# Kernel tuning notes

Hardware: AMD Instinct MI355X
Metric: run time of the kernel (lower is better)

Reference implementation:

```python
import jax, jax.numpy as jnp
import numpy as np

B, C, H, L, D = 128, 5, 50, 32, 300
VOCAB = 50000
KN = 20  # len(torch.arange(-0.9, 1.1, 0.1))
EPS = 1e-8


def setup_inputs() -> dict:
    key = jax.random.key(0)
    k1, k2, k3, k4 = jax.random.split(key, 4)
    return {
        "candidate_title": jax.random.randint(k1, (B, C, L), 0, VOCAB),
        "clicked_title": jax.random.randint(k2, (B, H, L), 0, VOCAB),
        "embedding": jax.random.normal(k3, (VOCAB, D), dtype=jnp.float32),
        "ltr_w": jax.random.normal(k4, (1, H * KN), dtype=jnp.float32) * 0.03,
        "ltr_b": jnp.zeros((1,), dtype=jnp.float32),
    }


def reference(candidate_title, clicked_title, embedding, ltr_w, ltr_b):
    mus = jnp.arange(KN, dtype=jnp.float32) * 0.1 - 0.9
    sigmas = jnp.concatenate([jnp.full((KN - 1,), 0.1, dtype=jnp.float32),
                              jnp.array([0.001], dtype=jnp.float32)])

    ce = embedding[candidate_title]            # [B,C,L,D]
    he = embedding[clicked_title]              # [B,H,L,D]
    # torch CosineSimilarity: dot / (clamp(||a||,eps)*clamp(||b||,eps))
    cn = ce / jnp.clip(jnp.linalg.norm(ce, axis=-1, keepdims=True), EPS)
    hn = he / jnp.clip(jnp.linalg.norm(he, axis=-1, keepdims=True), EPS)
    sim = jnp.einsum('bcid,bhjd->bchij', cn, hn)  # [B,C,H,L,L] fusion matrix

    # kernel pooling: sum over columns j per Gaussian kernel, then log-sum over rows i
    pooled = jnp.stack(
        [jnp.sum(jnp.exp(-(sim - mus[k]) ** 2 / (2.0 * sigmas[k] ** 2)), axis=-1)
         for k in range(KN)], axis=-1)          # [B,C,H,L,KN]
    pv = jnp.sum(jnp.log(jnp.clip(pooled, 1e-10)), axis=-2)  # [B,C,H,KN]
    pv = pv.reshape(B, C, H * KN)

    score = pv @ ltr_w.T + ltr_b               # [B,C,1]
    return jax.nn.log_softmax(score, axis=1)[..., 0]  # [B,C]
```

## Files before the change

kernel.cpp:

```cpp
#include <hip/hip_runtime.h>
#include <hip/hip_bf16.h>

#define VOCABN 50000
#define BN 128
#define CN 5
#define HN 50
#define LN 32
#define DN 300
#define DP 320
#define KNN 20

typedef __bf16    bf16x8 __attribute__((ext_vector_type(8)));
typedef float     f32x4  __attribute__((ext_vector_type(4)));
typedef float     f32x2  __attribute__((ext_vector_type(2)));
typedef ushort    u16x8  __attribute__((ext_vector_type(8)));

#if __has_builtin(__builtin_amdgcn_exp2f)
#define FEXP2 __builtin_amdgcn_exp2f
#else
#define FEXP2 exp2f
#endif
#if __has_builtin(__builtin_amdgcn_logf)
#define FLOG2 __builtin_amdgcn_logf
#else
#define FLOG2 log2f
#endif

#define LOG2E 1.4426950408889634f
#define LN2F  0.6931471805599453f

__global__ __launch_bounds__(256) void knorm_embed2(const float* __restrict__ emb,
                                                    ushort* __restrict__ tabo) {
    const int t    = threadIdx.x;
    const int lane = t & 63;
    const int w    = t >> 6;
    const int v    = blockIdx.x * 4 + w;
    const float* row = emb + (size_t)v * DN;
    const float4* r4 = (const float4*)row;

    float4 x = r4[lane];
    float ss = x.x * x.x + x.y * x.y + x.z * x.z + x.w * x.w;
    if (lane < 11) {
        float4 y = r4[64 + lane];
        ss += y.x * y.x + y.y * y.y + y.z * y.z + y.w * y.w;
    }
    #pragma unroll
    for (int off = 32; off; off >>= 1) ss += __shfl_xor(ss, off);
    const float scale = 1.0f / fmaxf(sqrtf(ss), 1e-8f);

    if (lane < 40) {
        u16x8 u;
        #pragma unroll
        for (int j = 0; j < 8; ++j) {
            int e = lane * 8 + j;
            float f = (e < DN) ? row[e] * scale : 0.f;
            __hip_bfloat16 h = __float2bfloat16(f);
            u[j] = *(ushort*)&h;
        }
        *(u16x8*)(tabo + (size_t)v * DP + lane * 8) = u;
    }
}

__device__ __forceinline__ int paddr(int row, int c) {
    return ((row >> 1) << 7) + ((((c + ((row & 1) << 2))) ^ ((row >> 1) & 7)) << 4);
}
__device__ __forceinline__ bf16x8 ldP(const ushort* buf, int row, int c) {
    return *(const bf16x8*)((const char*)buf + paddr(row, c));
}

__global__ __launch_bounds__(320, 6) void knrm_fused9(const int* __restrict__ cand,
                                                      const int* __restrict__ clik,
                                                      const ushort* __restrict__ tab,
                                                      const float* __restrict__ ltr_w,
                                                      float* __restrict__ score) {
    __shared__ __align__(16) char smem[25984];
    ushort* Bbuf0 = (ushort*)(smem + 21120);
    ushort* Bbuf1 = (ushort*)(smem + 23168);
    int*    tokA  = (int*)(smem + 25216);
    int*    tokB  = (int*)(smem + 25856);

    const int t    = threadIdx.x;
    const int lane = t & 63;
    const int w    = t >> 6;
    const int bid  = (blockIdx.x & 7) * 800 + (blockIdx.x >> 3);
    const int b    = bid / HN;
    const int h    = bid % HN;

    if (t < 160)      tokA[t] = cand[b * (CN * LN) + t];
    else if (t < 192) tokB[t - 160] = clik[b * (HN * LN) + h * LN + (t - 160)];
    __syncthreads();

    const int m15 = lane & 15;
    const int g4  = lane >> 4;

    const char* sA0 = (const char*)tab + (size_t)tokA[w * 32 + m15]      * (DP * 2) + g4 * 16;
    const char* sA1 = (const char*)tab + (size_t)tokA[w * 32 + 16 + m15] * (DP * 2) + g4 * 16;

    const char* srcB; int dstB;
    {
        int tb = t & 127;
        int ar = tb >> 2, c = tb & 3;
        srcB = (const char*)tab + (size_t)tokB[ar] * (DP * 2) + c * 16;
        dstB = paddr(ar, c);
    }

    f32x4 acc[2][2];
    #pragma unroll
    for (int at = 0; at < 2; ++at)
        #pragma unroll
        for (int jg = 0; jg < 2; ++jg)
            acc[at][jg] = (f32x4){0.f, 0.f, 0.f, 0.f};

    int4 bcur, bnext;
    if (t < 128) {
        int4 b0 = *(const int4*)(srcB);
        *(int4*)((char*)Bbuf0 + dstB) = b0;
        bcur = *(const int4*)(srcB + 64);
    }
    bf16x8 af0 = *(const bf16x8*)(sA0);
    bf16x8 af1 = *(const bf16x8*)(sA1);
    __syncthreads();

    #pragma unroll 2
    for (int ss = 0; ss < 10; ++ss) {
        const ushort* B = (ss & 1) ? Bbuf1 : Bbuf0;

        if (ss < 8 && t < 128) bnext = *(const int4*)(srcB + (ss + 2) * 64);
        bf16x8 an0 = af0, an1 = af1;
        if (ss < 9) {
            an0 = *(const bf16x8*)(sA0 + (ss + 1) * 64);
            an1 = *(const bf16x8*)(sA1 + (ss + 1) * 64);
        }

        bf16x8 bf0 = ldP(B, m15,      g4);
        bf16x8 bf1 = ldP(B, 16 + m15, g4);
        acc[0][0] = __builtin_amdgcn_mfma_f32_16x16x32_bf16(af0, bf0, acc[0][0], 0, 0, 0);
        acc[0][1] = __builtin_amdgcn_mfma_f32_16x16x32_bf16(af0, bf1, acc[0][1], 0, 0, 0);
        acc[1][0] = __builtin_amdgcn_mfma_f32_16x16x32_bf16(af1, bf0, acc[1][0], 0, 0, 0);
        acc[1][1] = __builtin_amdgcn_mfma_f32_16x16x32_bf16(af1, bf1, acc[1][1], 0, 0, 0);

        if (ss < 9) {
            if (t < 128) *(int4*)((char*)((ss & 1) ? Bbuf0 : Bbuf1) + dstB) = bcur;
            __syncthreads();
        }
        af0 = an0; af1 = an1;
        bcur = bnext;
    }
    __syncthreads();

    const float C1   = 10.0f * LOG2E;
    const float C2   = -50.0f * LOG2E;
    const float AK19 = 849.3218002880191f;
    static const float CkT[10] = {
        1.0f, 0.6065306597126334f, 0.1353352832366127f, 0.011108996538242306f,
        3.3546262790251185e-4f, 3.7266531720786709e-6f, 1.5229979744712628e-8f,
        2.2897348456191135e-11f, 1.2664165549094176e-14f, 2.576757109154981e-18f };

    float* sb = (float*)(smem + w * 4224);

    #pragma unroll
    for (int at = 0; at < 2; ++at)
        #pragma unroll
        for (int jgl = 0; jgl < 2; ++jgl)
            #pragma unroll
            for (int r = 0; r < 4; ++r)
                sb[(at * 16 + g4 * 4 + r) * 33 + jgl * 16 + m15] = acc[at][jgl][r];

    const int hi = lane >> 5;
    const float* sp = sb + (lane & 31) * 33 + hi * 16;

    f32x2 Qp[9];
    #pragma unroll
    for (int j = 0; j < 9; ++j) Qp[j] = (f32x2){0.f, 0.f};
    float Q9 = 0.f, Q19 = 0.f;

    #pragma unroll
    for (int ec = 0; ec < 4; ++ec) {
        f32x4 v = *(const f32x4*)(sp + ec * 4);
        #pragma unroll
        for (int e = 0; e < 4; ++e) {
            float s  = v[e];
            float cs = C1 * s;
            float tt = FEXP2(cs);
            float uu = FEXP2(-cs);
            float e0 = FEXP2(C2 * (s * s));
            Q9 += e0;
            f32x2 tu = {tt, uu};
            f32x2 pm = {e0, e0};
            #pragma unroll
            for (int j = 0; j < 9; ++j) { pm *= tu; Qp[j] += pm; }
            float d = fmaf(s, AK19, -AK19);
            Q19 += FEXP2(-(d * d));
        }
    }

    #pragma unroll
    for (int j = 0; j < 9; ++j) {
        Qp[j].x += __shfl_xor(Qp[j].x, 32);
        Qp[j].y += __shfl_xor(Qp[j].y, 32);
    }
    Q9  += __shfl_xor(Q9, 32);
    Q19 += __shfl_xor(Q19, 32);

    const float* wrow = ltr_w + h * KNN;
    float q0 = hi ? Q19 : Q9;
    float w0 = wrow[hi ? 19 : 9];
    float res = w0 * FLOG2(fmaxf(q0, 1e-10f));
    #pragma unroll
    for (int j = 1; j <= 9; ++j) {
        float q  = hi ? Qp[j - 1].x : Qp[j - 1].y;
        float wk = wrow[hi ? (9 + j) : (9 - j)];
        res += wk * FLOG2(fmaxf(q * CkT[j], 1e-10f));
    }

    res *= LN2F;
    #pragma unroll
    for (int off = 32; off; off >>= 1) res += __shfl_xor(res, off);
    if (lane == 0) atomicAdd(&score[b * CN + w], res);
}

__global__ __launch_bounds__(128) void knrm_final(const float* __restrict__ score,
                                                  float* __restrict__ out) {
    int b = threadIdx.x;
    if (b < BN) {
        float s[CN];
        float m = -1e30f;
        #pragma unroll
        for (int c = 0; c < CN; ++c) { s[c] = score[b * CN + c]; m = fmaxf(m, s[c]); }
        float sum = 0.f;
        #pragma unroll
        for (int c = 0; c < CN; ++c) sum += FEXP2((s[c] - m) * LOG2E);
        float lse = m + FLOG2(sum) * LN2F;
        #pragma unroll
        for (int c = 0; c < CN; ++c) out[b * CN + c] = s[c] - lse;
    }
}

extern "C" void kernel_launch(void* const* d_in, const int* in_sizes, int n_in,
                              void* d_out, int out_size, void* d_ws, size_t ws_size,
                              hipStream_t stream) {
    const int*   cand  = (const int*)d_in[0];
    const int*   clik  = (const int*)d_in[1];
    const float* emb   = (const float*)d_in[2];
    const float* ltr_w = (const float*)d_in[3];
    float* out = (float*)d_out;

    const size_t TAB_B = (size_t)VOCABN * DP * 2;

    ushort* tab  = (ushort*)d_ws;
    float*  scre = (float*)((char*)d_ws + TAB_B);

    hipMemsetAsync(scre, 0, BN * CN * sizeof(float), stream);
    knorm_embed2<<<VOCABN / 4, 256, 0, stream>>>(emb, tab);
    knrm_fused9<<<BN * HN, 320, 0, stream>>>(cand, clik, tab, ltr_w, scre);
    knrm_final<<<1, 128, 0, stream>>>(scre, out);
}
```

Measured before the change: 144.4 us.

## Load clicked-title B fragments directly from global instead of shared-memory double buffer

Each wave now loads its B operand fragments (the clicked-title rows) straight from the global/L2 table into registers, replacing the cooperative shared-memory double buffer. This removes the per-step __syncthreads barriers and LDS writes/reads, and the main loop is fully unrolled. The cost is that all five waves redundantly fetch the same B rows, which adds L1/L2 traffic and global-load latency to each step. Shared memory per block also shrinks.

```diff
diff --git a/kernel.cpp b/kernel.cpp
--- a/kernel.cpp
+++ b/kernel.cpp
@@ -61,23 +61,14 @@
     }
 }
 
-__device__ __forceinline__ int paddr(int row, int c) {
-    return ((row >> 1) << 7) + ((((c + ((row & 1) << 2))) ^ ((row >> 1) & 7)) << 4);
-}
-__device__ __forceinline__ bf16x8 ldP(const ushort* buf, int row, int c) {
-    return *(const bf16x8*)((const char*)buf + paddr(row, c));
-}
-
-__global__ __launch_bounds__(320, 6) void knrm_fused9(const int* __restrict__ cand,
-                                                      const int* __restrict__ clik,
-                                                      const ushort* __restrict__ tab,
-                                                      const float* __restrict__ ltr_w,
-                                                      float* __restrict__ score) {
-    __shared__ __align__(16) char smem[25984];
-    ushort* Bbuf0 = (ushort*)(smem + 21120);
-    ushort* Bbuf1 = (ushort*)(smem + 23168);
-    int*    tokA  = (int*)(smem + 25216);
-    int*    tokB  = (int*)(smem + 25856);
+__global__ __launch_bounds__(320, 6) void knrm_fused10(const int* __restrict__ cand,
+                                                       const int* __restrict__ clik,
+                                                       const ushort* __restrict__ tab,
+                                                       const float* __restrict__ ltr_w,
+                                                       float* __restrict__ score) {
+    __shared__ __align__(16) char smem[21888];
+    int* tokA = (int*)(smem + 21120);
+    int* tokB = (int*)(smem + 21760);
 
     const int t    = threadIdx.x;
     const int lane = t & 63;
@@ -95,14 +86,8 @@
 
     const char* sA0 = (const char*)tab + (size_t)tokA[w * 32 + m15]      * (DP * 2) + g4 * 16;
     const char* sA1 = (const char*)tab + (size_t)tokA[w * 32 + 16 + m15] * (DP * 2) + g4 * 16;
-
-    const char* srcB; int dstB;
-    {
-        int tb = t & 127;
-        int ar = tb >> 2, c = tb & 3;
-        srcB = (const char*)tab + (size_t)tokB[ar] * (DP * 2) + c * 16;
-        dstB = paddr(ar, c);
-    }
+    const char* sB0 = (const char*)tab + (size_t)tokB[m15]               * (DP * 2) + g4 * 16;
+    const char* sB1 = (const char*)tab + (size_t)tokB[16 + m15]          * (DP * 2) + g4 * 16;
 
     f32x4 acc[2][2];
     #pragma unroll
@@ -111,42 +96,26 @@
         for (int jg = 0; jg < 2; ++jg)
             acc[at][jg] = (f32x4){0.f, 0.f, 0.f, 0.f};
 
-    int4 bcur, bnext;
-    if (t < 128) {
-        int4 b0 = *(const int4*)(srcB);
-        *(int4*)((char*)Bbuf0 + dstB) = b0;
-        bcur = *(const int4*)(srcB + 64);
-    }
-    bf16x8 af0 = *(const bf16x8*)(sA0);
-    bf16x8 af1 = *(const bf16x8*)(sA1);
-    __syncthreads();
-
-    #pragma unroll 2
+    bf16x8 a0 = *(const bf16x8*)sA0;
+    bf16x8 a1 = *(const bf16x8*)sA1;
+    bf16x8 b0 = *(const bf16x8*)sB0;
+    bf16x8 b1 = *(const bf16x8*)sB1;
+
+    #pragma unroll
     for (int ss = 0; ss < 10; ++ss) {
-        const ushort* B = (ss & 1) ? Bbuf1 : Bbuf0;
-
-        if (ss < 8 && t < 128) bnext = *(const int4*)(srcB + (ss + 2) * 64);
-        bf16x8 an0 = af0, an1 = af1;
+        bf16x8 a0c = a0, a1c = a1, b0c = b0, b1c = b1;
         if (ss < 9) {
-            an0 = *(const bf16x8*)(sA0 + (ss + 1) * 64);
-            an1 = *(const bf16x8*)(sA1 + (ss + 1) * 64);
+            const int so = (ss + 1) * 64;
+            a0 = *(const bf16x8*)(sA0 + so);
+            a1 = *(const bf16x8*)(sA1 + so);
+            b0 = *(const bf16x8*)(sB0 + so);
+            b1 = *(const bf16x8*)(sB1 + so);
         }
-
-        bf16x8 bf0 = ldP(B, m15,      g4);
-        bf16x8 bf1 = ldP(B, 16 + m15, g4);
-        acc[0][0] = __builtin_amdgcn_mfma_f32_16x16x32_bf16(af0, bf0, acc[0][0], 0, 0, 0);
-        acc[0][1] = __builtin_amdgcn_mfma_f32_16x16x32_bf16(af0, bf1, acc[0][1], 0, 0, 0);
-        acc[1][0] = __builtin_amdgcn_mfma_f32_16x16x32_bf16(af1, bf0, acc[1][0], 0, 0, 0);
-        acc[1][1] = __builtin_amdgcn_mfma_f32_16x16x32_bf16(af1, bf1, acc[1][1], 0, 0, 0);
-
-        if (ss < 9) {
-            if (t < 128) *(int4*)((char*)((ss & 1) ? Bbuf0 : Bbuf1) + dstB) = bcur;
-            __syncthreads();
-        }
-        af0 = an0; af1 = an1;
-        bcur = bnext;
-    }
-    __syncthreads();
+        acc[0][0] = __builtin_amdgcn_mfma_f32_16x16x32_bf16(a0c, b0c, acc[0][0], 0, 0, 0);
+        acc[0][1] = __builtin_amdgcn_mfma_f32_16x16x32_bf16(a0c, b1c, acc[0][1], 0, 0, 0);
+        acc[1][0] = __builtin_amdgcn_mfma_f32_16x16x32_bf16(a1c, b0c, acc[1][0], 0, 0, 0);
+        acc[1][1] = __builtin_amdgcn_mfma_f32_16x16x32_bf16(a1c, b1c, acc[1][1], 0, 0, 0);
+    }
 
     const float C1   = 10.0f * LOG2E;
     const float C2   = -50.0f * LOG2E;
@@ -252,6 +221,6 @@
 
     hipMemsetAsync(scre, 0, BN * CN * sizeof(float), stream);
     knorm_embed2<<<VOCABN / 4, 256, 0, stream>>>(emb, tab);
-    knrm_fused9<<<BN * HN, 320, 0, stream>>>(cand, clik, tab, ltr_w, scre);
+    knrm_fused10<<<BN * HN, 320, 0, stream>>>(cand, clik, tab, ltr_w, scre);
     knrm_final<<<1, 128, 0, stream>>>(scre, out);
 }
```

New measurement: 196.6 us. 36.2% more time.
